# Performance work log

Measured on AMD Instinct MI355X. Metric: run time of the kernel, lower is better.

## Reference

```python
import jax, jax.numpy as jnp
import numpy as np

N = 100000   # nodes
E = 1600000  # edges
G = 256      # graphs in batch
C_IN = 128
D = 64
EPS = 1e-5
SLOPE = 0.01  # torch LeakyReLU default


def gcn_conv(h_x, src, dst, w_edge, W, b):
    """GCNConv: linear -> symmetric-normalized scatter aggregation (+ self loops) -> bias."""
    n = h_x.shape[0]
    h = h_x @ W                                   # [N, D]
    # add self loops with weight 1
    loop = jnp.arange(n, dtype=src.dtype)
    s = jnp.concatenate([src, loop])
    d = jnp.concatenate([dst, loop])
    w = jnp.concatenate([w_edge, jnp.ones((n,), h_x.dtype)])
    deg = jax.ops.segment_sum(w, d, num_segments=n)  # degree on target nodes
    dinv = jnp.where(deg > 0, jax.lax.rsqrt(jnp.maximum(deg, 1e-12)), 0.0)
    norm = dinv[s] * w * dinv[d]                  # [E+N]
    msg = h[s] * norm[:, None]                    # gather + scale
    out = jax.ops.segment_sum(msg, d, num_segments=n)
    return out + b


def batch_norm(h, gamma, beta):
    mean = jnp.mean(h, axis=0)
    var = jnp.mean((h - mean) ** 2, axis=0)       # biased var (training-mode BN)
    return (h - mean) * jax.lax.rsqrt(var + EPS) * gamma + beta


def setup_inputs() -> dict:
    key = jax.random.key(0)
    ks = jax.random.split(key, 16)
    inp = {
        "x": jax.random.normal(ks[0], (N, C_IN), jnp.float32),
        "edge_index": jax.random.randint(ks[1], (2, E), 0, N, jnp.int32),
        "batch": jnp.sort(jax.random.randint(ks[2], (N,), 0, G, jnp.int32)),
        "edge_attr": jax.random.uniform(ks[3], (E,), jnp.float32),
        "W0": jax.random.normal(ks[4], (C_IN, D), jnp.float32) * 0.05,
        "b0": jnp.zeros((D,), jnp.float32),
        "g0": jnp.ones((D,), jnp.float32),
        "be0": jnp.zeros((D,), jnp.float32),
        "W1": jax.random.normal(ks[5], (D, D), jnp.float32) * 0.05,
        "b1": jnp.zeros((D,), jnp.float32),
        "g1": jnp.ones((D,), jnp.float32),
        "be1": jnp.zeros((D,), jnp.float32),
        "W2": jax.random.normal(ks[6], (D, D), jnp.float32) * 0.05,
        "b2": jnp.zeros((D,), jnp.float32),
        "W3": jax.random.normal(ks[7], (D, D), jnp.float32) * 0.05,
        "b3": jnp.zeros((D,), jnp.float32),
        "Wfc": jax.random.normal(ks[8], (2 * D, 1), jnp.float32) * 0.05,
        "bfc": jnp.zeros((1,), jnp.float32),
    }
    return inp


def reference(x, edge_index, batch, edge_attr,
              W0, b0, g0, be0, W1, b1, g1, be1, W2, b2, W3, b3, Wfc, bfc):
    src, dst = edge_index[0], edge_index[1]
    lrelu = lambda h: jax.nn.leaky_relu(h, SLOPE)

    h = lrelu(batch_norm(gcn_conv(x, src, dst, edge_attr, W0, b0), g0, be0))
    h = lrelu(batch_norm(gcn_conv(h, src, dst, edge_attr, W1, b1), g1, be1))
    h = lrelu(gcn_conv(h, src, dst, edge_attr, W2, b2))  # dropout is identity in eval
    h = lrelu(gcn_conv(h, src, dst, edge_attr, W3, b3))

    mx = jax.ops.segment_max(h, batch, num_segments=G)
    sm = jax.ops.segment_sum(h, batch, num_segments=G)
    cnt = jax.ops.segment_sum(jnp.ones((N,), h.dtype), batch, num_segments=G)
    mean = sm / jnp.maximum(cnt, 1.0)[:, None]
    pooled = jnp.concatenate([mx, mean], axis=1)   # [G, 2D]
    return pooled @ Wfc + bfc                      # [G, 1]
```

## Files before the change

kernel.cpp:

```cpp
#include <hip/hip_runtime.h>
#include <math.h>

#define LRELU_SLOPE 0.01f
#define BN_EPS 1e-5f
#define WQ_SCALE 1048576.0f
#define WQ_INV   9.5367431640625e-7f

static inline int ceil_div(int a, int b) { return (a + b - 1) / b; }

typedef _Float16 f16;
typedef f16 h4_t __attribute__((ext_vector_type(4)));
typedef f16 h8_t __attribute__((ext_vector_type(8)));
typedef float f32x4 __attribute__((ext_vector_type(4)));

__device__ __forceinline__ unsigned short f2bf(float f) {
  unsigned int u = __float_as_uint(f);
  u = u + 0x7FFFu + ((u >> 16) & 1u);
  return (unsigned short)(u >> 16);
}
#define BF2F(u) __uint_as_float(((unsigned int)(u)) << 16)

__launch_bounds__(1024)
__global__ void b1_hist(const int* __restrict__ ei, int* __restrict__ histT,
                        int E, int chunk, int nbuck) {
  __shared__ unsigned int hist[1024];
  const int t = threadIdx.x;
  const int blk = blockIdx.x;
  hist[t] = 0;
  __syncthreads();
  const int e0 = blk * chunk;
  const int e1 = min(e0 + chunk, E);
  for (int e = e0 + t; e < e1; e += 1024) {
    int d = ei[E + e];
    atomicAdd(&hist[d >> 7], 1u);
  }
  __syncthreads();
  if (t < nbuck) histT[(size_t)t * 256 + blk] = (int)hist[t];
}

__global__ void scan1i(const int* __restrict__ in, int* __restrict__ out,
                       int* __restrict__ bsum, int n) {
  __shared__ int lds[256];
  const int t = threadIdx.x;
  const int base = blockIdx.x * 1024 + t * 4;
  int v0 = 0, v1 = 0, v2 = 0, v3 = 0;
  if (base + 0 < n) v0 = in[base + 0];
  if (base + 1 < n) v1 = in[base + 1];
  if (base + 2 < n) v2 = in[base + 2];
  if (base + 3 < n) v3 = in[base + 3];
  int s = v0 + v1 + v2 + v3;
  lds[t] = s;
  __syncthreads();
#pragma unroll
  for (int off = 1; off < 256; off <<= 1) {
    int y = 0;
    if (t >= off) y = lds[t - off];
    __syncthreads();
    if (t >= off) lds[t] += y;
    __syncthreads();
  }
  int incl = lds[t];
  int excl = incl - s;
  if (base + 0 < n) out[base + 0] = excl;
  if (base + 1 < n) out[base + 1] = excl + v0;
  if (base + 2 < n) out[base + 2] = excl + v0 + v1;
  if (base + 3 < n) out[base + 3] = excl + v0 + v1 + v2;
  if (t == 255) bsum[blockIdx.x] = incl;
}

__global__ void scan2i(int* __restrict__ bsum, int nb) {
  __shared__ int lds[256];
  int t = threadIdx.x;
  int v = (t < nb) ? bsum[t] : 0;
  lds[t] = v;
  __syncthreads();
#pragma unroll
  for (int off = 1; off < 256; off <<= 1) {
    int y = 0;
    if (t >= off) y = lds[t - off];
    __syncthreads();
    if (t >= off) lds[t] += y;
    __syncthreads();
  }
  if (t < nb) bsum[t] = lds[t] - v;
}

__global__ void scan3i(int* __restrict__ data, const int* __restrict__ bscan, int n) {
  int i = blockIdx.x * blockDim.x + threadIdx.x;
  if (i < n) data[i] += bscan[i >> 10];
}

__launch_bounds__(1024)
__global__ void b3_scatter(const int* __restrict__ ei, const float* __restrict__ w,
                           const int* __restrict__ histS,
                           unsigned long long* __restrict__ bucketed,
                           int E, int chunk, int nbuck) {
  __shared__ unsigned int cursor[1024];
  const int t = threadIdx.x;
  const int blk = blockIdx.x;
  cursor[t] = (t < nbuck) ? (unsigned int)histS[(size_t)t * 256 + blk] : 0u;
  __syncthreads();
  const int e0 = blk * chunk;
  const int e1 = min(e0 + chunk, E);
  for (int e = e0 + t; e < e1; e += 1024) {
    int s = ei[e];
    int d = ei[E + e];
    unsigned int pos = atomicAdd(&cursor[d >> 7], 1u);
    unsigned long long p = ((unsigned long long)(unsigned int)(d & 127) << 57) |
                           ((unsigned long long)(unsigned int)s << 32) |
                           (unsigned long long)__float_as_uint(w[e]);
    bucketed[pos] = p;
  }
}

__launch_bounds__(256)
__global__ void c1_degree(const unsigned long long* __restrict__ bucketed,
                          const int* __restrict__ histS,
                          int* __restrict__ rowstart, float* __restrict__ dinv,
                          int N, int E, int nbuck) {
  __shared__ unsigned int cnt[128], wsum[128];
  __shared__ int sc[128];
  const int t = threadIdx.x;
  const int b = blockIdx.x;
  if (t < 128) { cnt[t] = 0; wsum[t] = 0; }
  __syncthreads();
  const int r0 = histS[(size_t)b * 256];
  const int r1 = (b + 1 < nbuck) ? histS[(size_t)(b + 1) * 256] : E;
  for (int r = r0 + t; r < r1; r += 256) {
    unsigned long long p = bucketed[r];
    int d7 = (int)(p >> 57);
    float wv = __uint_as_float((unsigned int)p);
    atomicAdd(&cnt[d7], 1u);
    atomicAdd(&wsum[d7], (unsigned int)__float2uint_rn(wv * WQ_SCALE));
  }
  __syncthreads();
  if (t < 128) sc[t] = (int)cnt[t];
  __syncthreads();
#pragma unroll
  for (int off = 1; off < 128; off <<= 1) {
    int y = 0;
    if (t < 128 && t >= off) y = sc[t - off];
    __syncthreads();
    if (t < 128 && t >= off) sc[t] += y;
    __syncthreads();
  }
  if (t < 128) {
    int node = (b << 7) + t;
    if (node < N) {
      rowstart[node] = r0 + sc[t] - (int)cnt[t];
      float deg = 1.0f + (float)wsum[t] * WQ_INV;
      dinv[node] = rsqrtf(deg);
    }
  }
  if (b == 0 && t == 0) rowstart[N] = E;
}

__launch_bounds__(256)
__global__ void c2_fill(const unsigned long long* __restrict__ bucketed,
                        const int* __restrict__ histS,
                        const int* __restrict__ rowstart, const float* __restrict__ dinv,
                        unsigned long long* __restrict__ colval,
                        int N, int E, int nbuck) {
  __shared__ unsigned int cursor[128];
  const int t = threadIdx.x;
  const int b = blockIdx.x;
  if (t < 128) {
    int node = (b << 7) + t;
    cursor[t] = (node < N) ? (unsigned int)rowstart[node] : 0u;
  }
  __syncthreads();
  const int r0 = histS[(size_t)b * 256];
  const int r1 = (b + 1 < nbuck) ? histS[(size_t)(b + 1) * 256] : E;
  for (int r = r0 + t; r < r1; r += 256) {
    unsigned long long p = bucketed[r];
    int d7 = (int)(p >> 57);
    int s = (int)((p >> 32) & 0x1FFFFFF);
    float wv = __uint_as_float((unsigned int)p);
    unsigned int pos = atomicAdd(&cursor[d7], 1u);
    float v = wv * dinv[s];
    colval[pos] = ((unsigned long long)(unsigned int)s << 32) |
                  (unsigned long long)__float_as_uint(v);
  }
}

template <int K, int BN, int IN16>
__launch_bounds__(256, 4)
__global__ void k_gemm(const void* __restrict__ Xv, const float* __restrict__ W,
                       unsigned short* __restrict__ H16,
                       const float* __restrict__ s, const float* __restrict__ ss,
                       const float* __restrict__ g, const float* __restrict__ be,
                       int N) {
  constexpr int KP = K + 8;
  constexpr int KQ = K / 4;
  __shared__ f16 Xl[64 * KP];
  __shared__ f16 Wt[64 * KP];
  __shared__ float scaleC[64], shiftC[64];
  const int t = threadIdx.x;
  const int n0 = blockIdx.x * 64;

  if (BN) {
    if (t < 64) {
      float invN = 1.0f / (float)N;
      float mean = s[t] * invN;
      float var = ss[t] * invN - mean * mean;
      float sc = g[t] * rsqrtf(var + BN_EPS);
      scaleC[t] = sc;
      shiftC[t] = be[t] - mean * sc;
    }
    __syncthreads();
  }

  for (int idx = t; idx < 64 * KQ; idx += 256) {
    int row = idx / KQ;
    int kq = idx % KQ;
    int gn = n0 + row;
    float4 v = make_float4(0.f, 0.f, 0.f, 0.f);
    if (gn < N) {
      if (IN16) {
        ushort4 u = *(const ushort4*)((const unsigned short*)Xv + (size_t)gn * K + 4 * kq);
        v = make_float4(BF2F(u.x), BF2F(u.y), BF2F(u.z), BF2F(u.w));
      } else {
        v = *(const float4*)((const float*)Xv + (size_t)gn * K + 4 * kq);
      }
    }
    if (BN) {
      int c = 4 * kq;
      float a;
      a = v.x * scaleC[c + 0] + shiftC[c + 0]; v.x = (a > 0.f) ? a : LRELU_SLOPE * a;
      a = v.y * scaleC[c + 1] + shiftC[c + 1]; v.y = (a > 0.f) ? a : LRELU_SLOPE * a;
      a = v.z * scaleC[c + 2] + shiftC[c + 2]; v.z = (a > 0.f) ? a : LRELU_SLOPE * a;
      a = v.w * scaleC[c + 3] + shiftC[c + 3]; v.w = (a > 0.f) ? a : LRELU_SLOPE * a;
    }
    h4_t hv = { (f16)v.x, (f16)v.y, (f16)v.z, (f16)v.w };
    *(h4_t*)(Xl + row * KP + 4 * kq) = hv;
  }
  for (int idx = t; idx < K * 16; idx += 256) {
    int k = idx >> 4;
    int c4 = idx & 15;
    float4 wv = *(const float4*)(W + (size_t)k * 64 + 4 * c4);
    Wt[(4 * c4 + 0) * KP + k] = (f16)wv.x;
    Wt[(4 * c4 + 1) * KP + k] = (f16)wv.y;
    Wt[(4 * c4 + 2) * KP + k] = (f16)wv.z;
    Wt[(4 * c4 + 3) * KP + k] = (f16)wv.w;
  }
  __syncthreads();

  const int lane = t & 63;
  const int wv = t >> 6;
  const int fr = lane & 15;
  const int fc = lane >> 4;

  f32x4 acc0 = {0.f, 0.f, 0.f, 0.f};
  f32x4 acc1 = {0.f, 0.f, 0.f, 0.f};
  f32x4 acc2 = {0.f, 0.f, 0.f, 0.f};
  f32x4 acc3 = {0.f, 0.f, 0.f, 0.f};

  const f16* ap = Xl + (16 * wv + fr) * KP + 8 * fc;
  const f16* bp0 = Wt + (0 + fr) * KP + 8 * fc;
  const f16* bp1 = Wt + (16 + fr) * KP + 8 * fc;
  const f16* bp2 = Wt + (32 + fr) * KP + 8 * fc;
  const f16* bp3 = Wt + (48 + fr) * KP + 8 * fc;

#pragma unroll
  for (int kt = 0; kt < K; kt += 32) {
    h8_t a = *(const h8_t*)(ap + kt);
    acc0 = __builtin_amdgcn_mfma_f32_16x16x32_f16(a, *(const h8_t*)(bp0 + kt), acc0, 0, 0, 0);
    acc1 = __builtin_amdgcn_mfma_f32_16x16x32_f16(a, *(const h8_t*)(bp1 + kt), acc1, 0, 0, 0);
    acc2 = __builtin_amdgcn_mfma_f32_16x16x32_f16(a, *(const h8_t*)(bp2 + kt), acc2, 0, 0, 0);
    acc3 = __builtin_amdgcn_mfma_f32_16x16x32_f16(a, *(const h8_t*)(bp3 + kt), acc3, 0, 0, 0);
  }

#pragma unroll
  for (int r = 0; r < 4; ++r) {
    int node = n0 + 16 * wv + 4 * fc + r;
    if (node < N) {
      size_t base = (size_t)node * 64 + fr;
      H16[base + 0]  = f2bf(acc0[r]);
      H16[base + 16] = f2bf(acc1[r]);
      H16[base + 32] = f2bf(acc2[r]);
      H16[base + 48] = f2bf(acc3[r]);
    }
  }
}

#define AGG_GATH(cv) (*(const ushort4*)(h16 + ((size_t)((cv) >> 32)) * 64 + lane * 4))
#define AGG_FMA(a, cv, h)                                     \
  {                                                           \
    float v_ = __uint_as_float((unsigned int)(cv));           \
    (a).x += v_ * BF2F((h).x); (a).y += v_ * BF2F((h).y);     \
    (a).z += v_ * BF2F((h).z); (a).w += v_ * BF2F((h).w);     \
  }
template <int STATS, int LRELU, int OUT16>
__launch_bounds__(256)
__global__ void k_agg(const unsigned short* __restrict__ h16, void* __restrict__ hout,
                      const float* __restrict__ bias, const float* __restrict__ dinv,
                      const int* __restrict__ rowstart,
                      const unsigned long long* __restrict__ colval,
                      float* __restrict__ partial, int N) {
  __shared__ float4 rs[STATS ? 256 : 1];
  __shared__ float4 rq[STATS ? 256 : 1];
  const int t = threadIdx.x;
  const int grp = t >> 4;
  const int lane = t & 15;
  const int d = blockIdx.x * 16 + grp;
  const bool valid = (d < N);
  int r0 = 0, r1 = 0;
  if (valid) { r0 = rowstart[d]; r1 = rowstart[d + 1]; }
  float4 a0 = make_float4(0.f, 0.f, 0.f, 0.f);
  float4 a1 = make_float4(0.f, 0.f, 0.f, 0.f);
  float4 a2 = make_float4(0.f, 0.f, 0.f, 0.f);
  float4 a3 = make_float4(0.f, 0.f, 0.f, 0.f);
  int r = r0;
  for (; r + 8 <= r1; r += 8) {
    unsigned long long cv0 = colval[r + 0];
    unsigned long long cv1 = colval[r + 1];
    unsigned long long cv2 = colval[r + 2];
    unsigned long long cv3 = colval[r + 3];
    unsigned long long cv4 = colval[r + 4];
    unsigned long long cv5 = colval[r + 5];
    unsigned long long cv6 = colval[r + 6];
    unsigned long long cv7 = colval[r + 7];
    ushort4 h0 = AGG_GATH(cv0);
    ushort4 h1 = AGG_GATH(cv1);
    ushort4 h2 = AGG_GATH(cv2);
    ushort4 h3 = AGG_GATH(cv3);
    ushort4 h4 = AGG_GATH(cv4);
    ushort4 h5 = AGG_GATH(cv5);
    ushort4 h6 = AGG_GATH(cv6);
    ushort4 h7 = AGG_GATH(cv7);
    AGG_FMA(a0, cv0, h0); AGG_FMA(a1, cv1, h1);
    AGG_FMA(a2, cv2, h2); AGG_FMA(a3, cv3, h3);
    AGG_FMA(a0, cv4, h4); AGG_FMA(a1, cv5, h5);
    AGG_FMA(a2, cv6, h6); AGG_FMA(a3, cv7, h7);
  }
  for (; r + 4 <= r1; r += 4) {
    unsigned long long cv0 = colval[r + 0];
    unsigned long long cv1 = colval[r + 1];
    unsigned long long cv2 = colval[r + 2];
    unsigned long long cv3 = colval[r + 3];
    ushort4 h0 = AGG_GATH(cv0);
    ushort4 h1 = AGG_GATH(cv1);
    ushort4 h2 = AGG_GATH(cv2);
    ushort4 h3 = AGG_GATH(cv3);
    AGG_FMA(a0, cv0, h0); AGG_FMA(a1, cv1, h1);
    AGG_FMA(a2, cv2, h2); AGG_FMA(a3, cv3, h3);
  }
  for (; r < r1; ++r) {
    unsigned long long cv = colval[r];
    ushort4 hv = AGG_GATH(cv);
    AGG_FMA(a0, cv, hv);
  }
  float4 acc;
  acc.x = (a0.x + a1.x) + (a2.x + a3.x);
  acc.y = (a0.y + a1.y) + (a2.y + a3.y);
  acc.z = (a0.z + a1.z) + (a2.z + a3.z);
  acc.w = (a0.w + a1.w) + (a2.w + a3.w);
  float di = valid ? dinv[d] : 0.f;
  float di2 = di * di;
  ushort4 hd4 = make_ushort4(0, 0, 0, 0);
  if (valid) hd4 = *(const ushort4*)(h16 + (size_t)d * 64 + lane * 4);
  float4 b4 = *(const float4*)(bias + lane * 4);
  float4 o;
  o.x = di * acc.x + di2 * BF2F(hd4.x) + b4.x;
  o.y = di * acc.y + di2 * BF2F(hd4.y) + b4.y;
  o.z = di * acc.z + di2 * BF2F(hd4.z) + b4.z;
  o.w = di * acc.w + di2 * BF2F(hd4.w) + b4.w;
  if (LRELU) {
    o.x = (o.x > 0.f) ? o.x : LRELU_SLOPE * o.x;
    o.y = (o.y > 0.f) ? o.y : LRELU_SLOPE * o.y;
    o.z = (o.z > 0.f) ? o.z : LRELU_SLOPE * o.z;
    o.w = (o.w > 0.f) ? o.w : LRELU_SLOPE * o.w;
  }
  if (!valid) o = make_float4(0.f, 0.f, 0.f, 0.f);
  if (valid) {
    if (OUT16) {
      ushort4 o16;
      o16.x = f2bf(o.x); o16.y = f2bf(o.y); o16.z = f2bf(o.z); o16.w = f2bf(o.w);
      *(ushort4*)((unsigned short*)hout + (size_t)d * 64 + lane * 4) = o16;
    } else {
      *(float4*)((float*)hout + (size_t)d * 64 + lane * 4) = o;
    }
  }

  if (STATS) {
    rs[t] = o;
    rq[t] = make_float4(o.x * o.x, o.y * o.y, o.z * o.z, o.w * o.w);
    __syncthreads();
#pragma unroll
    for (int st = 8; st >= 1; st >>= 1) {
      if ((t >> 4) < st) {
        float4 sa = rs[t], sb = rs[t + st * 16];
        float4 qa = rq[t], qb = rq[t + st * 16];
        rs[t] = make_float4(sa.x + sb.x, sa.y + sb.y, sa.z + sb.z, sa.w + sb.w);
        rq[t] = make_float4(qa.x + qb.x, qa.y + qb.y, qa.z + qb.z, qa.w + qb.w);
      }
      __syncthreads();
    }
    if (t < 16) {
      float4 sv = rs[t], qv = rq[t];
      float* ps = partial + (size_t)blockIdx.x * 128 + 4 * t;
      ps[0] = sv.x; ps[1] = sv.y; ps[2] = sv.z; ps[3] = sv.w;
      ps[64] = qv.x; ps[65] = qv.y; ps[66] = qv.z; ps[67] = qv.w;
    }
  }
}

__global__ void k_stats_reduce(const float* __restrict__ partial, float* __restrict__ s,
                               float* __restrict__ ss, int nb) {
  __shared__ float red[256];
  const int c = blockIdx.x;
  const int t = threadIdx.x;
  float a = 0.f;
  for (int b = t; b < nb; b += 256) a += partial[(size_t)b * 128 + c];
  red[t] = a;
  __syncthreads();
  for (int st = 128; st >= 1; st >>= 1) {
    if (t < st) red[t] += red[t + st];
    __syncthreads();
  }
  if (t == 0) {
    if (c < 64) s[c] = red[0];
    else ss[c - 64] = red[0];
  }
}

__global__ void k_gbounds(const int* __restrict__ batch, int* __restrict__ gstart,
                          int N, int G) {
  int i = blockIdx.x * blockDim.x + threadIdx.x;
  if (i >= N) return;
  int b = batch[i];
  int prev = (i == 0) ? -1 : batch[i - 1];
  for (int g = prev + 1; g <= b; ++g) gstart[g] = i;
  if (i == N - 1) {
    for (int g = b + 1; g <= G; ++g) gstart[g] = N;
  }
}

__launch_bounds__(256)
__global__ void k_pool(const float* __restrict__ h, const int* __restrict__ gstart,
                       const float* __restrict__ Wfc, const float* __restrict__ bfc,
                       float* __restrict__ out, int G) {
  __shared__ float lmx[256], lsm[256], red[128];
  const int g = blockIdx.x;
  const int t = threadIdx.x;
  const int c = t & 63;
  const int sub = t >> 6;
  const int n0 = gstart[g];
  const int n1 = gstart[g + 1];
  float mx = -INFINITY, sm = 0.f;
  for (int n = n0 + sub; n < n1; n += 4) {
    float v = h[(size_t)n * 64 + c];
    mx = fmaxf(mx, v);
    sm += v;
  }
  lmx[t] = mx;
  lsm[t] = sm;
  __syncthreads();
  if (t < 64) {
    mx = fmaxf(fmaxf(lmx[t], lmx[t + 64]), fmaxf(lmx[t + 128], lmx[t + 192]));
    sm = lsm[t] + lsm[t + 64] + lsm[t + 128] + lsm[t + 192];
    float cntf = (float)(n1 - n0);
    float mean = sm / fmaxf(cntf, 1.0f);
    red[t] = mx * Wfc[t];
    red[t + 64] = mean * Wfc[64 + t];
  }
  __syncthreads();
  for (int st = 64; st >= 1; st >>= 1) {
    if (t < st) red[t] += red[t + st];
    __syncthreads();
  }
  if (t == 0) out[g] = red[0] + bfc[0];
}

extern "C" void kernel_launch(void* const* d_in, const int* in_sizes, int n_in,
                              void* d_out, int out_size, void* d_ws, size_t ws_size,
                              hipStream_t stream) {
  const float* x = (const float*)d_in[0];
  const int* ei = (const int*)d_in[1];
  const int* batch = (const int*)d_in[2];
  const float* eattr = (const float*)d_in[3];
  const float* W0 = (const float*)d_in[4];
  const float* b0 = (const float*)d_in[5];
  const float* g0 = (const float*)d_in[6];
  const float* be0 = (const float*)d_in[7];
  const float* W1 = (const float*)d_in[8];
  const float* b1 = (const float*)d_in[9];
  const float* g1 = (const float*)d_in[10];
  const float* be1 = (const float*)d_in[11];
  const float* W2 = (const float*)d_in[12];
  const float* b2 = (const float*)d_in[13];
  const float* W3 = (const float*)d_in[14];
  const float* b3 = (const float*)d_in[15];
  const float* Wfc = (const float*)d_in[16];
  const float* bfc = (const float*)d_in[17];
  float* out = (float*)d_out;

  const int N = in_sizes[2];
  const int E = in_sizes[3];
  const int CIN = in_sizes[0] / N;
  const int G = out_size;
  const int nbuck = ceil_div(N, 128);
  const int chunk = ceil_div(E, 256);
  const int M = nbuck * 256;
  const int nag = ceil_div(N, 16);

  size_t off = 0;
  auto alloc = [&](size_t bytes) -> void* {
    void* p = (char*)d_ws + off;
    off += (bytes + 255) & ~(size_t)255;
    return p;
  };
  int* histT = (int*)alloc((size_t)1024 * 256 * 4);
  int* histS = (int*)alloc((size_t)1024 * 256 * 4);
  int* bsum = (int*)alloc(1024 * 4);
  unsigned long long* bucketed = (unsigned long long*)alloc((size_t)E * 8);
  float* dinv = (float*)alloc((size_t)N * 4);
  int* rowstart = (int*)alloc((size_t)(N + 1) * 4);
  unsigned long long* colval = (unsigned long long*)alloc((size_t)E * 8);
  unsigned short* A16 = (unsigned short*)alloc((size_t)N * 64 * 2);
  unsigned short* B16 = (unsigned short*)alloc((size_t)N * 64 * 2);
  float* A = (float*)alloc((size_t)N * 64 * 4);
  unsigned short* H16 = (unsigned short*)alloc((size_t)N * 64 * 2);
  float* sums = (float*)alloc(256 * 4);
  float* partial = (float*)alloc((size_t)nag * 128 * 4);
  int* gstart = (int*)alloc((size_t)(G + 1) * 4);
  (void)ws_size; (void)n_in; (void)CIN;

  b1_hist<<<256, 1024, 0, stream>>>(ei, histT, E, chunk, nbuck);
  const int nbs = ceil_div(M, 1024);
  scan1i<<<nbs, 256, 0, stream>>>(histT, histS, bsum, M);
  scan2i<<<1, 256, 0, stream>>>(bsum, nbs);
  scan3i<<<ceil_div(M, 256), 256, 0, stream>>>(histS, bsum, M);
  b3_scatter<<<256, 1024, 0, stream>>>(ei, eattr, histS, bucketed, E, chunk, nbuck);
  c1_degree<<<nbuck, 256, 0, stream>>>(bucketed, histS, rowstart, dinv, N, E, nbuck);
  c2_fill<<<nbuck, 256, 0, stream>>>(bucketed, histS, rowstart, dinv, colval, N, E, nbuck);
  k_gbounds<<<ceil_div(N, 256), 256, 0, stream>>>(batch, gstart, N, G);

  k_gemm<128, 0, 0><<<ceil_div(N, 64), 256, 0, stream>>>(x, W0, H16, nullptr, nullptr, nullptr, nullptr, N);
  k_agg<1, 0, 1><<<nag, 256, 0, stream>>>(H16, B16, b0, dinv, rowstart, colval, partial, N);
  k_stats_reduce<<<128, 256, 0, stream>>>(partial, sums + 0, sums + 64, nag);

  k_gemm<64, 1, 1><<<ceil_div(N, 64), 256, 0, stream>>>(B16, W1, H16, sums + 0, sums + 64, g0, be0, N);
  k_agg<1, 0, 1><<<nag, 256, 0, stream>>>(H16, A16, b1, dinv, rowstart, colval, partial, N);
  k_stats_reduce<<<128, 256, 0, stream>>>(partial, sums + 128, sums + 192, nag);

  k_gemm<64, 1, 1><<<ceil_div(N, 64), 256, 0, stream>>>(A16, W2, H16, sums + 128, sums + 192, g1, be1, N);
  k_agg<0, 1, 1><<<nag, 256, 0, stream>>>(H16, B16, b2, dinv, rowstart, colval, nullptr, N);

  k_gemm<64, 0, 1><<<ceil_div(N, 64), 256, 0, stream>>>(B16, W3, H16, nullptr, nullptr, nullptr, nullptr, N);
  k_agg<0, 1, 0><<<nag, 256, 0, stream>>>(H16, A, b3, dinv, rowstart, colval, nullptr, N);

  k_pool<<<G, 256, 0, stream>>>(A, gstart, Wfc, bfc, out, G);
}
```

Baseline: 420.9 us.

## Sort destination nodes by degree for load-balanced aggregation

Adds a counting sort of nodes by in-degree (a histogram, a scan and a scatter) that produces an order array. The aggregation kernels then process nodes in that order, so each block's 16 node groups have similar degrees, which is meant to cut warp divergence and tail imbalance in the gather loop. The cost is seven extra small kernel launches, an indirection load per node, and scattered output writes that are no longer in node order.

```diff
diff --git a/kernel.cpp b/kernel.cpp
--- a/kernel.cpp
+++ b/kernel.cpp
@@ -180,6 +180,41 @@
     float v = wv * dinv[s];
     colval[pos] = ((unsigned long long)(unsigned int)s << 32) |
                   (unsigned long long)__float_as_uint(v);
+  }
+}
+
+__launch_bounds__(256)
+__global__ void d1_hist(const int* __restrict__ rowstart, int* __restrict__ histT,
+                        int N, int chunk) {
+  __shared__ unsigned int hist[256];
+  const int t = threadIdx.x;
+  const int blk = blockIdx.x;
+  hist[t] = 0;
+  __syncthreads();
+  const int i0 = blk * chunk;
+  const int i1 = min(i0 + chunk, N);
+  for (int i = i0 + t; i < i1; i += 256) {
+    int deg = rowstart[i + 1] - rowstart[i];
+    atomicAdd(&hist[min(deg, 255)], 1u);
+  }
+  __syncthreads();
+  histT[(size_t)t * 256 + blk] = (int)hist[t];
+}
+
+__launch_bounds__(256)
+__global__ void d3_scatter(const int* __restrict__ rowstart, const int* __restrict__ histS,
+                           int* __restrict__ order, int N, int chunk) {
+  __shared__ unsigned int cursor[256];
+  const int t = threadIdx.x;
+  const int blk = blockIdx.x;
+  cursor[t] = (unsigned int)histS[(size_t)t * 256 + blk];
+  __syncthreads();
+  const int i0 = blk * chunk;
+  const int i1 = min(i0 + chunk, N);
+  for (int i = i0 + t; i < i1; i += 256) {
+    int deg = rowstart[i + 1] - rowstart[i];
+    unsigned int pos = atomicAdd(&cursor[min(deg, 255)], 1u);
+    order[pos] = i;
   }
 }
 
@@ -296,14 +331,16 @@
                       const float* __restrict__ bias, const float* __restrict__ dinv,
                       const int* __restrict__ rowstart,
                       const unsigned long long* __restrict__ colval,
+                      const int* __restrict__ order,
                       float* __restrict__ partial, int N) {
   __shared__ float4 rs[STATS ? 256 : 1];
   __shared__ float4 rq[STATS ? 256 : 1];
   const int t = threadIdx.x;
   const int grp = t >> 4;
   const int lane = t & 15;
-  const int d = blockIdx.x * 16 + grp;
-  const bool valid = (d < N);
+  const int idx = blockIdx.x * 16 + grp;
+  const bool valid = (idx < N);
+  const int d = valid ? order[idx] : 0;
   int r0 = 0, r1 = 0;
   if (valid) { r0 = rowstart[d]; r1 = rowstart[d + 1]; }
   float4 a0 = make_float4(0.f, 0.f, 0.f, 0.f);
@@ -501,6 +538,7 @@
   const int G = out_size;
   const int nbuck = ceil_div(N, 128);
   const int chunk = ceil_div(E, 256);
+  const int chunkN = ceil_div(N, 256);
   const int M = nbuck * 256;
   const int nag = ceil_div(N, 16);
 
@@ -517,6 +555,7 @@
   float* dinv = (float*)alloc((size_t)N * 4);
   int* rowstart = (int*)alloc((size_t)(N + 1) * 4);
   unsigned long long* colval = (unsigned long long*)alloc((size_t)E * 8);
+  int* order = (int*)alloc((size_t)N * 4);
   unsigned short* A16 = (unsigned short*)alloc((size_t)N * 64 * 2);
   unsigned short* B16 = (unsigned short*)alloc((size_t)N * 64 * 2);
   float* A = (float*)alloc((size_t)N * 64 * 4);
@@ -534,21 +573,28 @@
   b3_scatter<<<256, 1024, 0, stream>>>(ei, eattr, histS, bucketed, E, chunk, nbuck);
   c1_degree<<<nbuck, 256, 0, stream>>>(bucketed, histS, rowstart, dinv, N, E, nbuck);
   c2_fill<<<nbuck, 256, 0, stream>>>(bucketed, histS, rowstart, dinv, colval, N, E, nbuck);
+  d1_hist<<<256, 256, 0, stream>>>(rowstart, histT, N, chunkN);
+  const int M2 = 256 * 256;
+  const int nbs2 = ceil_div(M2, 1024);
+  scan1i<<<nbs2, 256, 0, stream>>>(histT, histS, bsum, M2);
+  scan2i<<<1, 256, 0, stream>>>(bsum, nbs2);
+  scan3i<<<ceil_div(M2, 256), 256, 0, stream>>>(histS, bsum, M2);
+  d3_scatter<<<256, 256, 0, stream>>>(rowstart, histS, order, N, chunkN);
   k_gbounds<<<ceil_div(N, 256), 256, 0, stream>>>(batch, gstart, N, G);
 
   k_gemm<128, 0, 0><<<ceil_div(N, 64), 256, 0, stream>>>(x, W0, H16, nullptr, nullptr, nullptr, nullptr, N);
-  k_agg<1, 0, 1><<<nag, 256, 0, stream>>>(H16, B16, b0, dinv, rowstart, colval, partial, N);
+  k_agg<1, 0, 1><<<nag, 256, 0, stream>>>(H16, B16, b0, dinv, rowstart, colval, order, partial, N);
   k_stats_reduce<<<128, 256, 0, stream>>>(partial, sums + 0, sums + 64, nag);
 
   k_gemm<64, 1, 1><<<ceil_div(N, 64), 256, 0, stream>>>(B16, W1, H16, sums + 0, sums + 64, g0, be0, N);
-  k_agg<1, 0, 1><<<nag, 256, 0, stream>>>(H16, A16, b1, dinv, rowstart, colval, partial, N);
+  k_agg<1, 0, 1><<<nag, 256, 0, stream>>>(H16, A16, b1, dinv, rowstart, colval, order, partial, N);
   k_stats_reduce<<<128, 256, 0, stream>>>(partial, sums + 128, sums + 192, nag);
 
   k_gemm<64, 1, 1><<<ceil_div(N, 64), 256, 0, stream>>>(A16, W2, H16, sums + 128, sums + 192, g1, be1, N);
-  k_agg<0, 1, 1><<<nag, 256, 0, stream>>>(H16, B16, b2, dinv, rowstart, colval, nullptr, N);
+  k_agg<0, 1, 1><<<nag, 256, 0, stream>>>(H16, B16, b2, dinv, rowstart, colval, order, nullptr, N);
 
   k_gemm<64, 0, 1><<<ceil_div(N, 64), 256, 0, stream>>>(B16, W3, H16, nullptr, nullptr, nullptr, nullptr, N);
-  k_agg<0, 1, 0><<<nag, 256, 0, stream>>>(H16, A, b3, dinv, rowstart, colval, nullptr, N);
+  k_agg<0, 1, 0><<<nag, 256, 0, stream>>>(H16, A, b3, dinv, rowstart, colval, order, nullptr, N);
 
   k_pool<<<G, 256, 0, stream>>>(A, gstart, Wfc, bfc, out, G);
 }
```

Measured after the change: 436.5 us. 3.7% more time.

## Fuse CSR degree and fill kernels; fold source dinv scaling into GEMM epilogue

Applied to the files above, without the earlier changes.

Merges the degree/rowstart kernel and the CSR fill kernel into one pass over each bucket, so the bucketed edge list is read once fewer and one launch is dropped. The per-edge gather of dinv[src] is removed from CSR construction. Instead the GEMM epilogue pre-scales each output row by dinv[node], and the aggregation's self-loop term becomes di*(acc+h[d]). The cost is one extra dinv load per row in every GEMM, plus bf16 rounding now applied to pre-scaled features.

```diff
diff --git a/kernel.cpp b/kernel.cpp
--- a/kernel.cpp
+++ b/kernel.cpp
@@ -114,11 +114,12 @@
 }
 
 __launch_bounds__(256)
-__global__ void c1_degree(const unsigned long long* __restrict__ bucketed,
-                          const int* __restrict__ histS,
-                          int* __restrict__ rowstart, float* __restrict__ dinv,
-                          int N, int E, int nbuck) {
-  __shared__ unsigned int cnt[128], wsum[128];
+__global__ void c_build(const unsigned long long* __restrict__ bucketed,
+                        const int* __restrict__ histS,
+                        int* __restrict__ rowstart, float* __restrict__ dinv,
+                        unsigned long long* __restrict__ colval,
+                        int N, int E, int nbuck) {
+  __shared__ unsigned int cnt[128], wsum[128], cursor[128];
   __shared__ int sc[128];
   const int t = threadIdx.x;
   const int b = blockIdx.x;
@@ -146,47 +147,29 @@
   }
   if (t < 128) {
     int node = (b << 7) + t;
+    int rst = r0 + sc[t] - (int)cnt[t];
+    cursor[t] = (unsigned int)rst;
     if (node < N) {
-      rowstart[node] = r0 + sc[t] - (int)cnt[t];
+      rowstart[node] = rst;
       float deg = 1.0f + (float)wsum[t] * WQ_INV;
       dinv[node] = rsqrtf(deg);
     }
   }
-  if (b == 0 && t == 0) rowstart[N] = E;
-}
-
-__launch_bounds__(256)
-__global__ void c2_fill(const unsigned long long* __restrict__ bucketed,
-                        const int* __restrict__ histS,
-                        const int* __restrict__ rowstart, const float* __restrict__ dinv,
-                        unsigned long long* __restrict__ colval,
-                        int N, int E, int nbuck) {
-  __shared__ unsigned int cursor[128];
-  const int t = threadIdx.x;
-  const int b = blockIdx.x;
-  if (t < 128) {
-    int node = (b << 7) + t;
-    cursor[t] = (node < N) ? (unsigned int)rowstart[node] : 0u;
-  }
-  __syncthreads();
-  const int r0 = histS[(size_t)b * 256];
-  const int r1 = (b + 1 < nbuck) ? histS[(size_t)(b + 1) * 256] : E;
+  __syncthreads();
   for (int r = r0 + t; r < r1; r += 256) {
     unsigned long long p = bucketed[r];
     int d7 = (int)(p >> 57);
-    int s = (int)((p >> 32) & 0x1FFFFFF);
-    float wv = __uint_as_float((unsigned int)p);
     unsigned int pos = atomicAdd(&cursor[d7], 1u);
-    float v = wv * dinv[s];
-    colval[pos] = ((unsigned long long)(unsigned int)s << 32) |
-                  (unsigned long long)__float_as_uint(v);
-  }
+    colval[pos] = (p << 7) >> 7;
+  }
+  if (b == 0 && t == 0) rowstart[N] = E;
 }
 
 template <int K, int BN, int IN16>
 __launch_bounds__(256, 4)
 __global__ void k_gemm(const void* __restrict__ Xv, const float* __restrict__ W,
                        unsigned short* __restrict__ H16,
+                       const float* __restrict__ dinv,
                        const float* __restrict__ s, const float* __restrict__ ss,
                        const float* __restrict__ g, const float* __restrict__ be,
                        int N) {
@@ -274,11 +257,12 @@
   for (int r = 0; r < 4; ++r) {
     int node = n0 + 16 * wv + 4 * fc + r;
     if (node < N) {
+      float dv = dinv[node];
       size_t base = (size_t)node * 64 + fr;
-      H16[base + 0]  = f2bf(acc0[r]);
-      H16[base + 16] = f2bf(acc1[r]);
-      H16[base + 32] = f2bf(acc2[r]);
-      H16[base + 48] = f2bf(acc3[r]);
+      H16[base + 0]  = f2bf(acc0[r] * dv);
+      H16[base + 16] = f2bf(acc1[r] * dv);
+      H16[base + 32] = f2bf(acc2[r] * dv);
+      H16[base + 48] = f2bf(acc3[r] * dv);
     }
   }
 }
@@ -356,15 +340,14 @@
   acc.z = (a0.z + a1.z) + (a2.z + a3.z);
   acc.w = (a0.w + a1.w) + (a2.w + a3.w);
   float di = valid ? dinv[d] : 0.f;
-  float di2 = di * di;
   ushort4 hd4 = make_ushort4(0, 0, 0, 0);
   if (valid) hd4 = *(const ushort4*)(h16 + (size_t)d * 64 + lane * 4);
   float4 b4 = *(const float4*)(bias + lane * 4);
   float4 o;
-  o.x = di * acc.x + di2 * BF2F(hd4.x) + b4.x;
-  o.y = di * acc.y + di2 * BF2F(hd4.y) + b4.y;
-  o.z = di * acc.z + di2 * BF2F(hd4.z) + b4.z;
-  o.w = di * acc.w + di2 * BF2F(hd4.w) + b4.w;
+  o.x = di * (acc.x + BF2F(hd4.x)) + b4.x;
+  o.y = di * (acc.y + BF2F(hd4.y)) + b4.y;
+  o.z = di * (acc.z + BF2F(hd4.z)) + b4.z;
+  o.w = di * (acc.w + BF2F(hd4.w)) + b4.w;
   if (LRELU) {
     o.x = (o.x > 0.f) ? o.x : LRELU_SLOPE * o.x;
     o.y = (o.y > 0.f) ? o.y : LRELU_SLOPE * o.y;
@@ -532,22 +515,21 @@
   scan2i<<<1, 256, 0, stream>>>(bsum, nbs);
   scan3i<<<ceil_div(M, 256), 256, 0, stream>>>(histS, bsum, M);
   b3_scatter<<<256, 1024, 0, stream>>>(ei, eattr, histS, bucketed, E, chunk, nbuck);
-  c1_degree<<<nbuck, 256, 0, stream>>>(bucketed, histS, rowstart, dinv, N, E, nbuck);
-  c2_fill<<<nbuck, 256, 0, stream>>>(bucketed, histS, rowstart, dinv, colval, N, E, nbuck);
+  c_build<<<nbuck, 256, 0, stream>>>(bucketed, histS, rowstart, dinv, colval, N, E, nbuck);
   k_gbounds<<<ceil_div(N, 256), 256, 0, stream>>>(batch, gstart, N, G);
 
-  k_gemm<128, 0, 0><<<ceil_div(N, 64), 256, 0, stream>>>(x, W0, H16, nullptr, nullptr, nullptr, nullptr, N);
+  k_gemm<128, 0, 0><<<ceil_div(N, 64), 256, 0, stream>>>(x, W0, H16, dinv, nullptr, nullptr, nullptr, nullptr, N);
   k_agg<1, 0, 1><<<nag, 256, 0, stream>>>(H16, B16, b0, dinv, rowstart, colval, partial, N);
   k_stats_reduce<<<128, 256, 0, stream>>>(partial, sums + 0, sums + 64, nag);
 
-  k_gemm<64, 1, 1><<<ceil_div(N, 64), 256, 0, stream>>>(B16, W1, H16, sums + 0, sums + 64, g0, be0, N);
+  k_gemm<64, 1, 1><<<ceil_div(N, 64), 256, 0, stream>>>(B16, W1, H16, dinv, sums + 0, sums + 64, g0, be0, N);
   k_agg<1, 0, 1><<<nag, 256, 0, stream>>>(H16, A16, b1, dinv, rowstart, colval, partial, N);
   k_stats_reduce<<<128, 256, 0, stream>>>(partial, sums + 128, sums + 192, nag);
 
-  k_gemm<64, 1, 1><<<ceil_div(N, 64), 256, 0, stream>>>(A16, W2, H16, sums + 128, sums + 192, g1, be1, N);
+  k_gemm<64, 1, 1><<<ceil_div(N, 64), 256, 0, stream>>>(A16, W2, H16, dinv, sums + 128, sums + 192, g1, be1, N);
   k_agg<0, 1, 1><<<nag, 256, 0, stream>>>(H16, B16, b2, dinv, rowstart, colval, nullptr, N);
 
-  k_gemm<64, 0, 1><<<ceil_div(N, 64), 256, 0, stream>>>(B16, W3, H16, nullptr, nullptr, nullptr, nullptr, N);
+  k_gemm<64, 0, 1><<<ceil_div(N, 64), 256, 0, stream>>>(B16, W3, H16, dinv, nullptr, nullptr, nullptr, nullptr, N);
   k_agg<0, 1, 0><<<nag, 256, 0, stream>>>(H16, A, b3, dinv, rowstart, colval, nullptr, N);
 
   k_pool<<<G, 256, 0, stream>>>(A, gstart, Wfc, bfc, out, G);
```

Measured after the change: 419.5 us. Within noise of the previous version (-0.3%).
